# Kernel tuning notes

Hardware: AMD Instinct MI355X
Metric: run time of the kernel (lower is better)

## Reference

```python
import math
import jax, jax.numpy as jnp
import numpy as np

D_MODEL, D_HEAD, BLOCK, B, N = 1024, 128, 2048, 4, 2048
# mode_gate('wake') blend weights (omega_lang, omega_grav)
OMEGA_LANG, OMEGA_GRAV = 0.7, 0.3


def setup_inputs() -> dict:
    key = jax.random.key(0)
    kx, kq, kk, kv, kl = jax.random.split(key, 5)
    x = jax.random.normal(kx, (B, N, D_MODEL), dtype=jnp.float32)
    # nn.Linear(d_model, d_head, bias=False) -> store as [d_model, d_head] for x @ W
    s = 1.0 / math.sqrt(D_MODEL)
    Wq = jax.random.uniform(kq, (D_MODEL, D_HEAD), jnp.float32, -s, s)
    Wk = jax.random.uniform(kk, (D_MODEL, D_HEAD), jnp.float32, -s, s)
    Wv = jax.random.uniform(kv, (D_MODEL, D_HEAD), jnp.float32, -s, s)
    # L_grav = eye*0.3 + randn*0.05
    L_grav = jnp.eye(D_HEAD, dtype=jnp.float32) * 0.3 \
        + jax.random.normal(kl, (D_HEAD, D_HEAD), dtype=jnp.float32) * 0.05
    return {"x": x, "Wq": Wq, "Wk": Wk, "Wv": Wv, "L_grav": L_grav}


def reference(x, Wq, Wk, Wv, L_grav):
    b, n, _ = x.shape
    d_head = Wq.shape[1]
    q = x @ Wq          # [b, n, d]
    k = x @ Wk          # [b, n, d]
    v = x @ Wv          # [b, n, d]
    mask = jnp.tril(jnp.ones((n, n), dtype=bool))  # causal, broadcast over batch

    # lang_attention: scaled dot-product with causal softmax
    scores = jnp.einsum('bqd,bkd->bqk', q, k) / math.sqrt(d_head)
    scores = jnp.where(mask, scores, -jnp.inf)
    a_lang = jax.nn.softmax(scores, axis=-1)       # [b, n, n]

    # grav_attention: Gaussian kernel on Mahalanobis-transformed keys y = k @ L_grav,
    # sigma = sqrt(d_head); masked + row-normalized (non-softmax).
    y = k @ L_grav                                  # [b, n, d]
    sq = jnp.sum(y * y, axis=-1)                    # [b, n]
    gram = jnp.einsum('bqd,bkd->bqk', y, y)         # [b, n, n]
    dist2 = jnp.maximum(sq[:, :, None] + sq[:, None, :] - 2.0 * gram, 0.0)
    kern = jnp.exp(-dist2 / (2.0 * d_head))         # sigma^2 = d_head
    kern = jnp.where(mask, kern, 0.0)
    a_grav = kern / (jnp.sum(kern, axis=-1, keepdims=True) + 1e-8)

    a = OMEGA_LANG * a_lang + OMEGA_GRAV * a_grav   # mode='wake' gate blend
    return a @ v                                    # [b, n, d_head]
```

## Files before the change

### kernel.cpp

```cpp
#include <hip/hip_runtime.h>
#include <hip/hip_bf16.h>
#include <math.h>

typedef __attribute__((ext_vector_type(8))) short short8;
typedef __attribute__((ext_vector_type(4))) short s16x4;
typedef __attribute__((ext_vector_type(4))) float f32x4;

#define SEQ 2048
#define DH 128

__device__ __forceinline__ short f2bf(float f) {
    union { float f; unsigned u; } v; v.f = f;
    unsigned r = v.u + 0x7fffu + ((v.u >> 16) & 1u);
    return (short)(r >> 16);
}
__device__ __forceinline__ float bf2f(short s) {
    union { unsigned u; float f; } v; v.u = ((unsigned)(unsigned short)s) << 16;
    return v.f;
}

__device__ __forceinline__ void gll16(const void* g, void* l) {
    __builtin_amdgcn_global_load_lds(
        (const __attribute__((address_space(1))) unsigned int*)g,
        (__attribute__((address_space(3))) unsigned int*)l, 16, 0, 0);
}

__global__ __launch_bounds__(256) void wt_kernel(
    const float* __restrict__ Wq, const float* __restrict__ Wk, const float* __restrict__ Wv,
    short* __restrict__ Wt2)
{
    const int t = threadIdx.x;
    const int m  = blockIdx.x >> 4;
    const int ks = blockIdx.x & 15;
    const float* W = m == 0 ? Wq : (m == 1 ? Wk : Wv);
    short* dst = Wt2 + ((size_t)(m * 16 + ks) * 1024) * 8;
    #pragma unroll
    for (int j = 0; j < 4; j++) {
        const int idx = t * 4 + j;
        const int ctile = idx >> 7;
        const int kc = (idx >> 6) & 1;
        const int gg = (idx >> 4) & 3;
        const int cc = idx & 15;
        const int col = ctile * 16 + cc;
        const int kb = ks * 64 + kc * 32 + gg * 8;
        short8 h;
        #pragma unroll
        for (int e = 0; e < 8; e++) h[e] = f2bf(W[(size_t)(kb + e) * 128 + col]);
        *(short8*)&dst[idx * 8] = h;
    }
}

__global__ __launch_bounds__(256) void proj_kernel(
    const float* __restrict__ x, const short* __restrict__ Wt2,
    short* __restrict__ Qh, short* __restrict__ Kh, short* __restrict__ Vh)
{
    __shared__ short Xs[2048];
    __shared__ short Ws[8192];
    const int t = threadIdx.x;
    const int w = t >> 6, l = t & 63;
    const int c = l & 15, g = l >> 4;
    const int bid = blockIdx.x;
    const int m = bid % 3;
    const int row0 = (bid / 3) * 32;
    const short* Wm = Wt2 + (size_t)m * 16 * 1024 * 8;

    const int xr = t >> 3;
    const int xk = (t & 7) * 8;
    const int xIdx = ((xr >> 4) * 2 + (xk >> 5)) * 64 + ((xk >> 3) & 3) * 16 + (xr & 15);

    const int rt = w & 1;
    const int ct4 = (w >> 1) * 4;
    f32x4 acc[4];
    #pragma unroll
    for (int nt = 0; nt < 4; nt++) acc[nt] = (f32x4)0.f;

    for (int ks = 0; ks < 16; ks++) {
        __syncthreads();
        const short* wsrc = Wm + ((size_t)ks * 1024 + w * 256 + l) * 8;
        #pragma unroll
        for (int j = 0; j < 4; j++)
            gll16(wsrc + j * 64 * 8, (void*)&Ws[(w * 256 + j * 64) * 8]);
        {
            const float* xp = &x[(size_t)(row0 + xr) * 1024 + ks * 64 + xk];
            const float4 a = *(const float4*)xp;
            const float4 b = *(const float4*)(xp + 4);
            short8 h;
            h[0] = f2bf(a.x); h[1] = f2bf(a.y); h[2] = f2bf(a.z); h[3] = f2bf(a.w);
            h[4] = f2bf(b.x); h[5] = f2bf(b.y); h[6] = f2bf(b.z); h[7] = f2bf(b.w);
            *(short8*)&Xs[xIdx * 8] = h;
        }
        __syncthreads();
        #pragma unroll
        for (int kc = 0; kc < 2; kc++) {
            const short8 af = *(const short8*)&Xs[((rt * 2 + kc) * 64 + l) * 8];
            #pragma unroll
            for (int nt = 0; nt < 4; nt++) {
                const short8 bf = *(const short8*)&Ws[(((ct4 + nt) * 2 + kc) * 64 + l) * 8];
                acc[nt] = __builtin_amdgcn_mfma_f32_16x16x32_bf16(af, bf, acc[nt], 0, 0, 0);
            }
        }
    }
    short* Out = m == 0 ? Qh : (m == 1 ? Kh : Vh);
    #pragma unroll
    for (int nt = 0; nt < 4; nt++)
        #pragma unroll
        for (int r = 0; r < 4; r++)
            Out[(size_t)(row0 + rt * 16 + 4 * g + r) * 128 + (ct4 + nt) * 16 + c] = f2bf(acc[nt][r]);
}

__global__ __launch_bounds__(256) void y_kernel(
    const short* __restrict__ Kh, const float* __restrict__ L,
    short* __restrict__ Yh, float* __restrict__ SQ)
{
    __shared__ float Ls[128 * 128];
    __shared__ short Ks[16][128];
    const int t = threadIdx.x;
    const int row0 = blockIdx.x * 16;
    #pragma unroll
    for (int j = 0; j < 16; j++) {
        int lin = t + j * 256;
        ((float4*)Ls)[lin] = ((const float4*)L)[lin];
    }
    {
        int r = t >> 4, ch = t & 15;
        *(short8*)&Ks[r][ch * 8] = *(const short8*)&Kh[(size_t)(row0 + r) * 128 + ch * 8];
    }
    __syncthreads();
    const int rl = t >> 4, c4 = (t & 15) * 4;
    float acc[8] = {};
    for (int d = 0; d < 128; d++) {
        const float kd = bf2f(Ks[rl][d]);
        const float4 l0 = *(const float4*)&Ls[d * 128 + c4];
        const float4 l1 = *(const float4*)&Ls[d * 128 + c4 + 64];
        acc[0] += kd * l0.x; acc[1] += kd * l0.y; acc[2] += kd * l0.z; acc[3] += kd * l0.w;
        acc[4] += kd * l1.x; acc[5] += kd * l1.y; acc[6] += kd * l1.z; acc[7] += kd * l1.w;
    }
    const int row = row0 + rl;
    s16x4 h0, h1;
    float s = 0.f;
    #pragma unroll
    for (int j = 0; j < 4; j++) {
        short h = f2bf(acc[j]);     float rv = bf2f(h); s += rv * rv; h0[j] = h;
        short g = f2bf(acc[j + 4]); float gv = bf2f(g); s += gv * gv; h1[j] = g;
    }
    *(s16x4*)&Yh[(size_t)row * 128 + c4]      = h0;
    *(s16x4*)&Yh[(size_t)row * 128 + c4 + 64] = h1;
    for (int off = 1; off < 16; off <<= 1) s += __shfl_xor(s, off);
    if ((t & 15) == 0) SQ[row] = s;
}

__global__ __launch_bounds__(256) void vt_kernel(
    const short* __restrict__ Vh, short* __restrict__ Vt)
{
    __shared__ short Ls[64][72];
    const int t = threadIdx.x;
    const int b  = blockIdx.x >> 6;
    const int nb = (blockIdx.x >> 1) & 31;
    const int db = blockIdx.x & 1;
    const int n0 = nb * 64, d0 = db * 64;
    const short* Vb = Vh + (size_t)b * SEQ * 128;
    short* Vtb = Vt + (size_t)b * 128 * SEQ;
    #pragma unroll
    for (int i = 0; i < 2; i++) {
        int row = (t >> 3) + 32 * i;
        int ch = t & 7;
        *(short8*)&Ls[row][ch * 8] = *(const short8*)&Vb[(size_t)(n0 + row) * 128 + d0 + ch * 8];
    }
    __syncthreads();
    #pragma unroll
    for (int i = 0; i < 2; i++) {
        int dd = (t >> 3) + 32 * i;
        int nc = t & 7;
        short8 v;
        #pragma unroll
        for (int j = 0; j < 8; j++) v[j] = Ls[nc * 8 + j][dd];
        *(short8*)&Vtb[(size_t)(d0 + dd) * SEQ + n0 + nc * 8] = v;
    }
}

__global__ __launch_bounds__(64) void attn_kernel(
    const short* __restrict__ Qh, const short* __restrict__ Kh,
    const short* __restrict__ Yh, const short* __restrict__ Vt,
    const float* __restrict__ SQv,
    float* __restrict__ OL, float* __restrict__ OG,
    float* __restrict__ LS, float* __restrict__ GS)
{
    __shared__ short P[32 * 64];
    const int l = threadIdx.x;
    const int c = l & 15, g = l >> 4;
    const int bid = blockIdx.x;
    const int grav = bid >> 10;
    const int rest = bid & 1023;
    const int b = rest & 3;
    const int s = (rest >> 2) & 7;
    const int jp = rest >> 5;

    const size_t boff = (size_t)b * SEQ * 128;
    const short* Ab = (grav ? Yh : Qh) + boff;
    const short* Bb = (grav ? Yh : Kh) + boff;
    const short* Vb = Vt + boff;
    const float* SQb = SQv + b * SEQ;
    float* O  = grav ? OG : OL;
    float* RS = grav ? GS : LS;

    for (int m = 0; m < 2; m++) {
        const int qt = m ? 63 - jp : jp;
        const int q0 = qt * 32;
        const int nkt = (qt + 2) >> 1;

        short8 qf[2][4];
        #pragma unroll
        for (int mt = 0; mt < 2; mt++)
            #pragma unroll
            for (int kc = 0; kc < 4; kc++)
                qf[mt][kc] = *(const short8*)&Ab[(size_t)(q0 + mt * 16 + c) * 128 + kc * 32 + 8 * g];

        float sqq[2][4];
        if (grav) {
            #pragma unroll
            for (int mt = 0; mt < 2; mt++)
                #pragma unroll
                for (int r = 0; r < 4; r++)
                    sqq[mt][r] = SQb[q0 + mt * 16 + 4 * g + r];
        }

        f32x4 acc[2][8];
        #pragma unroll
        for (int mt = 0; mt < 2; mt++)
            #pragma unroll
            for (int dt = 0; dt < 8; dt++) acc[mt][dt] = (f32x4)0.f;
        float rsum[2][4] = {};

        for (int tt = s; tt < nkt; tt += 8) {
            const int k0 = tt * 64;
            #pragma unroll
            for (int kt = 0; kt < 4; kt++) {
                const int kbase = k0 + kt * 16;
                if (kbase <= q0 + 31) {
                    short8 bf[4];
                    #pragma unroll
                    for (int kc = 0; kc < 4; kc++)
                        bf[kc] = *(const short8*)&Bb[(size_t)(kbase + c) * 128 + kc * 32 + 8 * g];
                    const float sqk = grav ? SQb[kbase + c] : 0.f;
                    #pragma unroll
                    for (int mt = 0; mt < 2; mt++) {
                        f32x4 sc = (f32x4)0.f;
                        #pragma unroll
                        for (int kc = 0; kc < 4; kc++)
                            sc = __builtin_amdgcn_mfma_f32_16x16x32_bf16(qf[mt][kc], bf[kc], sc, 0, 0, 0);
                        #pragma unroll
                        for (int r = 0; r < 4; r++) {
                            const int qrow = q0 + mt * 16 + 4 * g + r;
                            const int key = kbase + c;
                            float p = 0.f;
                            if (key <= qrow) {
                                if (grav) {
                                    float d2 = sqq[mt][r] + sqk - 2.f * sc[r];
                                    d2 = fmaxf(d2, 0.f);
                                    p = __expf(d2 * -0.00390625f);
                                } else {
                                    p = __expf(sc[r] * 0.08838834764831845f);
                                }
                            }
                            const short ph = f2bf(p);
                            rsum[mt][r] += bf2f(ph);
                            const int row = mt * 16 + 4 * g + r;
                            P[((row * 128 + (kt * 16 + c) * 2) ^ ((row & 7) << 4)) >> 1] = ph;
                        }
                    }
                } else {
                    #pragma unroll
                    for (int mt = 0; mt < 2; mt++)
                        #pragma unroll
                        for (int r = 0; r < 4; r++) {
                            const int row = mt * 16 + 4 * g + r;
                            P[((row * 128 + (kt * 16 + c) * 2) ^ ((row & 7) << 4)) >> 1] = 0;
                        }
                }
            }
            __syncthreads();
            short8 pf[2][2];
            #pragma unroll
            for (int mt = 0; mt < 2; mt++)
                #pragma unroll
                for (int kc = 0; kc < 2; kc++) {
                    const int row = mt * 16 + c;
                    const int off = (row * 128 + 16 * g + 64 * kc) ^ ((row & 7) << 4);
                    pf[mt][kc] = *(const short8*)((const char*)P + off);
                }
            #pragma unroll
            for (int dt = 0; dt < 8; dt++) {
                #pragma unroll
                for (int kc = 0; kc < 2; kc++) {
                    const short8 vf = *(const short8*)&Vb[(size_t)(dt * 16 + c) * SEQ + k0 + kc * 32 + 8 * g];
                    #pragma unroll
                    for (int mt = 0; mt < 2; mt++)
                        acc[mt][dt] = __builtin_amdgcn_mfma_f32_16x16x32_bf16(pf[mt][kc], vf, acc[mt][dt], 0, 0, 0);
                }
            }
            __syncthreads();
        }

        #pragma unroll
        for (int mt = 0; mt < 2; mt++)
            #pragma unroll
            for (int r = 0; r < 4; r++) {
                float v = rsum[mt][r];
                v += __shfl_xor(v, 1); v += __shfl_xor(v, 2);
                v += __shfl_xor(v, 4); v += __shfl_xor(v, 8);
                rsum[mt][r] = v;
            }
        if (c == 0) {
            #pragma unroll
            for (int mt = 0; mt < 2; mt++)
                #pragma unroll
                for (int r = 0; r < 4; r++)
                    atomicAdd(&RS[b * SEQ + q0 + mt * 16 + 4 * g + r], rsum[mt][r]);
        }
        #pragma unroll
        for (int mt = 0; mt < 2; mt++)
            #pragma unroll
            for (int dt = 0; dt < 8; dt++)
                #pragma unroll
                for (int r = 0; r < 4; r++)
                    atomicAdd(&O[boff + (size_t)(q0 + mt * 16 + 4 * g + r) * 128 + dt * 16 + c],
                              acc[mt][dt][r]);
    }
}

__global__ __launch_bounds__(256) void finalize_kernel(
    float* __restrict__ out, const float* __restrict__ OG,
    const float* __restrict__ LS, const float* __restrict__ GS)
{
    const int i4 = blockIdx.x * 256 + threadIdx.x;
    float4 o = ((float4*)out)[i4];
    const float4 gv = ((const float4*)OG)[i4];
    const int row = i4 >> 5;
    const float wl = 0.7f / LS[row];
    const float wg = 0.3f / (GS[row] + 1e-8f);
    o.x = o.x * wl + gv.x * wg;
    o.y = o.y * wl + gv.y * wg;
    o.z = o.z * wl + gv.z * wg;
    o.w = o.w * wl + gv.w * wg;
    ((float4*)out)[i4] = o;
}

extern "C" void kernel_launch(void* const* d_in, const int* in_sizes, int n_in,
                              void* d_out, int out_size, void* d_ws, size_t ws_size,
                              hipStream_t stream) {
    const float* x  = (const float*)d_in[0];
    const float* Wq = (const float*)d_in[1];
    const float* Wk = (const float*)d_in[2];
    const float* Wv = (const float*)d_in[3];
    const float* Lg = (const float*)d_in[4];

    char* ws = (char*)d_ws;
    short* Qh  = (short*)(ws + 0);
    short* Kh  = (short*)(ws + 2097152);
    short* Vh  = (short*)(ws + 4194304);
    short* Yh  = (short*)(ws + 6291456);
    short* Vt  = (short*)(ws + 8388608);
    short* Wt2 = (short*)(ws + 10485760);
    float* SQv = (float*)(ws + 11272192);
    float* LS  = (float*)(ws + 11304960);
    float* GS  = (float*)(ws + 11337728);
    float* OG  = (float*)(ws + 11370496);
    float* OL  = (float*)d_out;

    hipMemsetAsync(d_out, 0, 4194304, stream);
    hipMemsetAsync((void*)LS, 0, 65536, stream);
    hipMemsetAsync((void*)OG, 0, 4194304, stream);

    wt_kernel<<<48, 256, 0, stream>>>(Wq, Wk, Wv, Wt2);
    proj_kernel<<<768, 256, 0, stream>>>(x, Wt2, Qh, Kh, Vh);
    y_kernel<<<512, 256, 0, stream>>>(Kh, Lg, Yh, SQv);
    vt_kernel<<<256, 256, 0, stream>>>(Vh, Vt);
    attn_kernel<<<2048, 64, 0, stream>>>(Qh, Kh, Yh, Vt, SQv, OL, OG, LS, GS);
    finalize_kernel<<<1024, 256, 0, stream>>>((float*)d_out, OG, LS, GS);
}
```

Before: 121.7 us.

## Reduce attention split-K partials in LDS within 4-wave blocks, drop memsets

The attention kernel now runs one 256-thread block per (query tile, batch, mode). Its four waves split the key tiles among themselves, and each wave uses its own P scratch buffer with only a wave-local LDS fence, so no block barriers are needed in the loop. Partial outputs and row sums are reduced through LDS atomics and written once with plain stores. This removes the global atomics and the three memsets. The cost is 4-way instead of 8-way key splitting, with longest-first tile ordering, so there are fewer blocks and long causal rows may cause load imbalance.

```diff
diff --git a/kernel.cpp b/kernel.cpp
--- a/kernel.cpp
+++ b/kernel.cpp
@@ -23,6 +23,11 @@
     __builtin_amdgcn_global_load_lds(
         (const __attribute__((address_space(1))) unsigned int*)g,
         (__attribute__((address_space(3))) unsigned int*)l, 16, 0, 0);
+}
+
+__device__ __forceinline__ void wave_lds_fence() {
+    asm volatile("s_waitcnt lgkmcnt(0)" ::: "memory");
+    __builtin_amdgcn_sched_barrier(0);
 }
 
 __global__ __launch_bounds__(256) void wt_kernel(
@@ -178,154 +183,164 @@
     }
 }
 
-__global__ __launch_bounds__(64) void attn_kernel(
+__global__ __launch_bounds__(256, 4) void attn_kernel(
     const short* __restrict__ Qh, const short* __restrict__ Kh,
     const short* __restrict__ Yh, const short* __restrict__ Vt,
     const float* __restrict__ SQv,
     float* __restrict__ OL, float* __restrict__ OG,
     float* __restrict__ LS, float* __restrict__ GS)
 {
-    __shared__ short P[32 * 64];
-    const int l = threadIdx.x;
+    __shared__ short P[4 * 2048];
+    __shared__ float Obuf[32][132];
+    __shared__ float Rs[32];
+    const int t = threadIdx.x;
+    const int w = t >> 6, l = t & 63;
     const int c = l & 15, g = l >> 4;
     const int bid = blockIdx.x;
-    const int grav = bid >> 10;
-    const int rest = bid & 1023;
-    const int b = rest & 3;
-    const int s = (rest >> 2) & 7;
-    const int jp = rest >> 5;
+    const int qt = 63 - (bid >> 3);
+    const int b = bid & 3;
+    const int grav = (bid >> 2) & 1;
+    const int q0 = qt * 32;
+    const int nkt = (qt + 2) >> 1;
+
+    for (int i = t; i < 32 * 132; i += 256) ((float*)Obuf)[i] = 0.f;
+    if (t < 32) Rs[t] = 0.f;
+    __syncthreads();
 
     const size_t boff = (size_t)b * SEQ * 128;
     const short* Ab = (grav ? Yh : Qh) + boff;
     const short* Bb = (grav ? Yh : Kh) + boff;
     const short* Vb = Vt + boff;
     const float* SQb = SQv + b * SEQ;
-    float* O  = grav ? OG : OL;
-    float* RS = grav ? GS : LS;
-
-    for (int m = 0; m < 2; m++) {
-        const int qt = m ? 63 - jp : jp;
-        const int q0 = qt * 32;
-        const int nkt = (qt + 2) >> 1;
-
-        short8 qf[2][4];
+    short* Pw = P + w * 2048;
+
+    short8 qf[2][4];
+    #pragma unroll
+    for (int mt = 0; mt < 2; mt++)
+        #pragma unroll
+        for (int kc = 0; kc < 4; kc++)
+            qf[mt][kc] = *(const short8*)&Ab[(size_t)(q0 + mt * 16 + c) * 128 + kc * 32 + 8 * g];
+
+    float sqq[2][4];
+    if (grav) {
         #pragma unroll
         for (int mt = 0; mt < 2; mt++)
             #pragma unroll
-            for (int kc = 0; kc < 4; kc++)
-                qf[mt][kc] = *(const short8*)&Ab[(size_t)(q0 + mt * 16 + c) * 128 + kc * 32 + 8 * g];
-
-        float sqq[2][4];
-        if (grav) {
-            #pragma unroll
-            for (int mt = 0; mt < 2; mt++)
+            for (int r = 0; r < 4; r++)
+                sqq[mt][r] = SQb[q0 + mt * 16 + 4 * g + r];
+    }
+
+    f32x4 acc[2][8];
+    #pragma unroll
+    for (int mt = 0; mt < 2; mt++)
+        #pragma unroll
+        for (int dt = 0; dt < 8; dt++) acc[mt][dt] = (f32x4)0.f;
+    float rsum[2][4] = {};
+
+    for (int tt = w; tt < nkt; tt += 4) {
+        const int k0 = tt * 64;
+        #pragma unroll
+        for (int kt = 0; kt < 4; kt++) {
+            const int kbase = k0 + kt * 16;
+            if (kbase <= q0 + 31) {
+                short8 bf[4];
                 #pragma unroll
-                for (int r = 0; r < 4; r++)
-                    sqq[mt][r] = SQb[q0 + mt * 16 + 4 * g + r];
-        }
-
-        f32x4 acc[2][8];
-        #pragma unroll
-        for (int mt = 0; mt < 2; mt++)
-            #pragma unroll
-            for (int dt = 0; dt < 8; dt++) acc[mt][dt] = (f32x4)0.f;
-        float rsum[2][4] = {};
-
-        for (int tt = s; tt < nkt; tt += 8) {
-            const int k0 = tt * 64;
-            #pragma unroll
-            for (int kt = 0; kt < 4; kt++) {
-                const int kbase = k0 + kt * 16;
-                if (kbase <= q0 + 31) {
-                    short8 bf[4];
+                for (int kc = 0; kc < 4; kc++)
+                    bf[kc] = *(const short8*)&Bb[(size_t)(kbase + c) * 128 + kc * 32 + 8 * g];
+                const float sqk = grav ? SQb[kbase + c] : 0.f;
+                #pragma unroll
+                for (int mt = 0; mt < 2; mt++) {
+                    f32x4 sc = (f32x4)0.f;
                     #pragma unroll
                     for (int kc = 0; kc < 4; kc++)
-                        bf[kc] = *(const short8*)&Bb[(size_t)(kbase + c) * 128 + kc * 32 + 8 * g];
-                    const float sqk = grav ? SQb[kbase + c] : 0.f;
+                        sc = __builtin_amdgcn_mfma_f32_16x16x32_bf16(qf[mt][kc], bf[kc], sc, 0, 0, 0);
                     #pragma unroll
-                    for (int mt = 0; mt < 2; mt++) {
-                        f32x4 sc = (f32x4)0.f;
-                        #pragma unroll
-                        for (int kc = 0; kc < 4; kc++)
-                            sc = __builtin_amdgcn_mfma_f32_16x16x32_bf16(qf[mt][kc], bf[kc], sc, 0, 0, 0);
-                        #pragma unroll
-                        for (int r = 0; r < 4; r++) {
-                            const int qrow = q0 + mt * 16 + 4 * g + r;
-                            const int key = kbase + c;
-                            float p = 0.f;
-                            if (key <= qrow) {
-                                if (grav) {
-                                    float d2 = sqq[mt][r] + sqk - 2.f * sc[r];
-                                    d2 = fmaxf(d2, 0.f);
-                                    p = __expf(d2 * -0.00390625f);
-                                } else {
-                                    p = __expf(sc[r] * 0.08838834764831845f);
-                                }
+                    for (int r = 0; r < 4; r++) {
+                        const int qrow = q0 + mt * 16 + 4 * g + r;
+                        const int key = kbase + c;
+                        float p = 0.f;
+                        if (key <= qrow) {
+                            if (grav) {
+                                float d2 = sqq[mt][r] + sqk - 2.f * sc[r];
+                                d2 = fmaxf(d2, 0.f);
+                                p = __expf(d2 * -0.00390625f);
+                            } else {
+                                p = __expf(sc[r] * 0.08838834764831845f);
                             }
-                            const short ph = f2bf(p);
-                            rsum[mt][r] += bf2f(ph);
-                            const int row = mt * 16 + 4 * g + r;
-                            P[((row * 128 + (kt * 16 + c) * 2) ^ ((row & 7) << 4)) >> 1] = ph;
                         }
+                        const short ph = f2bf(p);
+                        rsum[mt][r] += bf2f(ph);
+                        const int row = mt * 16 + 4 * g + r;
+                        Pw[((row * 128 + (kt * 16 + c) * 2) ^ ((row & 7) << 4)) >> 1] = ph;
                     }
-                } else {
+                }
+            } else {
+                #pragma unroll
+                for (int mt = 0; mt < 2; mt++)
                     #pragma unroll
-                    for (int mt = 0; mt < 2; mt++)
-                        #pragma unroll
-                        for (int r = 0; r < 4; r++) {
-                            const int row = mt * 16 + 4 * g + r;
-                            P[((row * 128 + (kt * 16 + c) * 2) ^ ((row & 7) << 4)) >> 1] = 0;
-                        }
-                }
+                    for (int r = 0; r < 4; r++) {
+                        const int row = mt * 16 + 4 * g + r;
+                        Pw[((row * 128 + (kt * 16 + c) * 2) ^ ((row & 7) << 4)) >> 1] = 0;
+                    }
             }
-            __syncthreads();
-            short8 pf[2][2];
-            #pragma unroll
-            for (int mt = 0; mt < 2; mt++)
+        }
+        wave_lds_fence();
+        short8 pf[2][2];
+        #pragma unroll
+        for (int mt = 0; mt < 2; mt++)
+            #pragma unroll
+            for (int kc = 0; kc < 2; kc++) {
+                const int row = mt * 16 + c;
+                const int off = (row * 128 + 16 * g + 64 * kc) ^ ((row & 7) << 4);
+                pf[mt][kc] = *(const short8*)((const char*)Pw + off);
+            }
+        #pragma unroll
+        for (int dt = 0; dt < 8; dt++) {
+            #pragma unroll
+            for (int kc = 0; kc < 2; kc++) {
+                const short8 vf = *(const short8*)&Vb[(size_t)(dt * 16 + c) * SEQ + k0 + kc * 32 + 8 * g];
                 #pragma unroll
-                for (int kc = 0; kc < 2; kc++) {
-                    const int row = mt * 16 + c;
-                    const int off = (row * 128 + 16 * g + 64 * kc) ^ ((row & 7) << 4);
-                    pf[mt][kc] = *(const short8*)((const char*)P + off);
-                }
-            #pragma unroll
-            for (int dt = 0; dt < 8; dt++) {
-                #pragma unroll
-                for (int kc = 0; kc < 2; kc++) {
-                    const short8 vf = *(const short8*)&Vb[(size_t)(dt * 16 + c) * SEQ + k0 + kc * 32 + 8 * g];
-                    #pragma unroll
-                    for (int mt = 0; mt < 2; mt++)
-                        acc[mt][dt] = __builtin_amdgcn_mfma_f32_16x16x32_bf16(pf[mt][kc], vf, acc[mt][dt], 0, 0, 0);
-                }
+                for (int mt = 0; mt < 2; mt++)
+                    acc[mt][dt] = __builtin_amdgcn_mfma_f32_16x16x32_bf16(pf[mt][kc], vf, acc[mt][dt], 0, 0, 0);
             }
-            __syncthreads();
-        }
-
+        }
+        wave_lds_fence();
+    }
+
+    #pragma unroll
+    for (int mt = 0; mt < 2; mt++)
+        #pragma unroll
+        for (int dt = 0; dt < 8; dt++)
+            #pragma unroll
+            for (int r = 0; r < 4; r++)
+                atomicAdd(&Obuf[mt * 16 + 4 * g + r][dt * 16 + c], acc[mt][dt][r]);
+
+    #pragma unroll
+    for (int mt = 0; mt < 2; mt++)
+        #pragma unroll
+        for (int r = 0; r < 4; r++) {
+            float v = rsum[mt][r];
+            v += __shfl_xor(v, 1); v += __shfl_xor(v, 2);
+            v += __shfl_xor(v, 4); v += __shfl_xor(v, 8);
+            rsum[mt][r] = v;
+        }
+    if (c == 0) {
         #pragma unroll
         for (int mt = 0; mt < 2; mt++)
             #pragma unroll
-            for (int r = 0; r < 4; r++) {
-                float v = rsum[mt][r];
-                v += __shfl_xor(v, 1); v += __shfl_xor(v, 2);
-                v += __shfl_xor(v, 4); v += __shfl_xor(v, 8);
-                rsum[mt][r] = v;
-            }
-        if (c == 0) {
-            #pragma unroll
-            for (int mt = 0; mt < 2; mt++)
-                #pragma unroll
-                for (int r = 0; r < 4; r++)
-                    atomicAdd(&RS[b * SEQ + q0 + mt * 16 + 4 * g + r], rsum[mt][r]);
-        }
-        #pragma unroll
-        for (int mt = 0; mt < 2; mt++)
-            #pragma unroll
-            for (int dt = 0; dt < 8; dt++)
-                #pragma unroll
-                for (int r = 0; r < 4; r++)
-                    atomicAdd(&O[boff + (size_t)(q0 + mt * 16 + 4 * g + r) * 128 + dt * 16 + c],
-                              acc[mt][dt][r]);
-    }
+            for (int r = 0; r < 4; r++)
+                atomicAdd(&Rs[mt * 16 + 4 * g + r], rsum[mt][r]);
+    }
+    __syncthreads();
+
+    float* Op = (grav ? OG : OL) + boff + (size_t)q0 * 128;
+    #pragma unroll
+    for (int i = 0; i < 4; i++) {
+        const int v = t + 256 * i;
+        const int row = v >> 5, c4 = (v & 31) * 4;
+        *(float4*)&Op[row * 128 + c4] = *(const float4*)&Obuf[row][c4];
+    }
+    if (t < 32) (grav ? GS : LS)[b * SEQ + q0 + t] = Rs[t];
 }
 
 __global__ __launch_bounds__(256) void finalize_kernel(
@@ -367,14 +382,10 @@
     float* OG  = (float*)(ws + 11370496);
     float* OL  = (float*)d_out;
 
-    hipMemsetAsync(d_out, 0, 4194304, stream);
-    hipMemsetAsync((void*)LS, 0, 65536, stream);
-    hipMemsetAsync((void*)OG, 0, 4194304, stream);
-
     wt_kernel<<<48, 256, 0, stream>>>(Wq, Wk, Wv, Wt2);
     proj_kernel<<<768, 256, 0, stream>>>(x, Wt2, Qh, Kh, Vh);
     y_kernel<<<512, 256, 0, stream>>>(Kh, Lg, Yh, SQv);
     vt_kernel<<<256, 256, 0, stream>>>(Vh, Vt);
-    attn_kernel<<<2048, 64, 0, stream>>>(Qh, Kh, Yh, Vt, SQv, OL, OG, LS, GS);
+    attn_kernel<<<512, 256, 0, stream>>>(Qh, Kh, Yh, Vt, SQv, OL, OG, LS, GS);
     finalize_kernel<<<1024, 256, 0, stream>>>((float*)d_out, OG, LS, GS);
 }
```

Result: slower. 213.1 us (+75.1%).
